# Performance work log

Measured on AMD Instinct MI355X. Metric: run time of the kernel, lower is better.

The kernel has to match this reference:

```python
import jax, jax.numpy as jnp
import numpy as np

B, S, E, L = 8, 2048, 512, 128


def setup_inputs() -> dict:
    key = jax.random.key(0)
    k1, k2 = jax.random.split(key)
    embeddings = jax.random.normal(k1, (B, S, E), dtype=jnp.float32)
    means = jax.random.normal(k2, (L, E), dtype=jnp.float32)
    var = jnp.ones((E,), dtype=jnp.float32)  # default init: requires_grad=False, ones
    return {"embeddings": embeddings, "means": means, "var": var}


def reference(embeddings, means, var):
    # Diagonal-Gaussian log-density per (token, label):
    #   log_density - 0.5 * sum_e (means[l,e] - emb[b,s,e])^2 / var[e]
    # Rewritten as GEMM + per-row/per-label norms (avoids [B,S,L,E] intermediate).
    n_embed = embeddings.shape[-1]
    factor = -n_embed / 2.0 * (np.log(2.0) + np.log(np.pi))
    # After init_params: log_density = factor - 0.5 * sum(log var); var=ones -> factor.
    log_density = factor - 0.5 * jnp.sum(jnp.log(var))
    inv_var = 1.0 / var  # [E]
    e2 = jnp.einsum('bse,e->bs', embeddings * embeddings, inv_var)      # [B,S]
    m2 = jnp.einsum('le,e->l', means * means, inv_var)                  # [L]
    cross = jnp.einsum('bse,le->bsl', embeddings, means * inv_var)      # [B,S,L]
    sq_mahalanobis = e2[..., None] + m2[None, None, :] - 2.0 * cross    # [B,S,L]
    return log_density - 0.5 * sq_mahalanobis
```

## Files before the change

### kernel.cpp

```cpp
#include <hip/hip_runtime.h>
#include <math.h>

#define BDIM 8
#define SDIM 2048
#define EDIM 512
#define LDIM 128
#define MTOT (BDIM * SDIM)
#define TM 32
#define BK 64
#define PAD 8
#define LSTR (BK + PAD)

typedef __attribute__((ext_vector_type(8))) short s8v;
typedef __attribute__((ext_vector_type(4))) float f4v;

__device__ __forceinline__ unsigned short f2bf(float x) {
    union { float f; unsigned u; } c; c.f = x;
    return (unsigned short)((c.u + 0x7fffu + ((c.u >> 16) & 1u)) >> 16);
}

__global__ __launch_bounds__(64) void gs_prep(
    const float* __restrict__ means, const float* __restrict__ var,
    unsigned short* __restrict__ Bmat, float* __restrict__ m2,
    float* __restrict__ ivbuf, float* __restrict__ coef)
{
    const int l = blockIdx.x;
    const int t = threadIdx.x;
    const int e0 = t * 8;

    float mv[8], iv[8];
    const float* mrow = means + l * EDIM + e0;
#pragma unroll
    for (int i = 0; i < 8; ++i) { mv[i] = mrow[i]; iv[i] = 1.0f / var[e0 + i]; }

    float part = 0.0f;
    s8v pr;
#pragma unroll
    for (int i = 0; i < 8; ++i) {
        float p = mv[i] * iv[i];
        pr[i] = (short)f2bf(p);
        part += mv[i] * p;
    }
    *(s8v*)(Bmat + l * EDIM + e0) = pr;

#pragma unroll
    for (int off = 32; off > 0; off >>= 1) part += __shfl_down(part, off, 64);
    if (t == 0) m2[l] = part;

    if (l == 0) {
#pragma unroll
        for (int i = 0; i < 8; ++i) ivbuf[e0 + i] = iv[i];
        float ld = 0.0f;
#pragma unroll
        for (int i = 0; i < 8; ++i) ld += logf(var[e0 + i]);
#pragma unroll
        for (int off = 32; off > 0; off >>= 1) ld += __shfl_down(ld, off, 64);
        if (t == 0) {
            const float factor = -(float)EDIM * 0.5f * 1.8378770664093453f;
            *coef = factor - 0.5f * ld;
        }
    }
}

__global__ __launch_bounds__(256) void gs_main(
    const float* __restrict__ emb, const unsigned short* __restrict__ Bmat,
    const float* __restrict__ m2, const float* __restrict__ ivbuf,
    const float* __restrict__ coef, float* __restrict__ out)
{
    __shared__ __align__(16) unsigned short Alds[TM][LSTR];
    __shared__ __align__(16) unsigned short Blds[LDIM][LSTR];
    __shared__ float e2part[256];
    __shared__ float e2s[TM];

    const int t    = threadIdx.x;
    const int lane = t & 63;
    const int wave = t >> 6;
    const int m0   = blockIdx.x * TM;

    const int arow = t >> 3;
    const int kseg = (t & 7) * 8;

    const int r0w  = (wave >> 1) * 16;
    const int c0w  = (wave & 1) * 64;
    const int frow = lane & 15;
    const int fk   = (lane >> 4) * 8;

    f4v acc[4];
#pragma unroll
    for (int i = 0; i < 4; ++i) acc[i] = (f4v)0.0f;

    float e2acc = 0.0f;
    const float* embp = emb + (m0 + arow) * EDIM + kseg;
    const unsigned short* bp = Bmat + arow * EDIM + kseg;

    for (int kc = 0; kc < EDIM / BK; ++kc) {
        const int k0 = kc * BK;
        f4v x0 = *(const f4v*)(embp + k0);
        f4v x1 = *(const f4v*)(embp + k0 + 4);
        f4v v0 = *(const f4v*)(ivbuf + k0 + kseg);
        f4v v1 = *(const f4v*)(ivbuf + k0 + kseg + 4);
        s8v b0 = *(const s8v*)(bp + (0 * 32) * EDIM + k0);
        s8v b1 = *(const s8v*)(bp + (1 * 32) * EDIM + k0);
        s8v b2 = *(const s8v*)(bp + (2 * 32) * EDIM + k0);
        s8v b3 = *(const s8v*)(bp + (3 * 32) * EDIM + k0);

        s8v a8;
#pragma unroll
        for (int i = 0; i < 4; ++i) {
            a8[i] = (short)f2bf(x0[i]);
            e2acc += x0[i] * x0[i] * v0[i];
        }
#pragma unroll
        for (int i = 0; i < 4; ++i) {
            a8[4 + i] = (short)f2bf(x1[i]);
            e2acc += x1[i] * x1[i] * v1[i];
        }

        __syncthreads();
        *(s8v*)&Alds[arow][kseg] = a8;
        *(s8v*)&Blds[arow +  0][kseg] = b0;
        *(s8v*)&Blds[arow + 32][kseg] = b1;
        *(s8v*)&Blds[arow + 64][kseg] = b2;
        *(s8v*)&Blds[arow + 96][kseg] = b3;
        __syncthreads();

#pragma unroll
        for (int ks = 0; ks < BK; ks += 32) {
            s8v af = *(const s8v*)&Alds[r0w + frow][ks + fk];
#pragma unroll
            for (int ct = 0; ct < 4; ++ct) {
                s8v bfv = *(const s8v*)&Blds[c0w + ct * 16 + frow][ks + fk];
                acc[ct] = __builtin_amdgcn_mfma_f32_16x16x32_bf16(af, bfv, acc[ct], 0, 0, 0);
            }
        }
    }

    e2part[t] = e2acc;
    __syncthreads();
    if (t < TM) {
        float s = 0.0f;
#pragma unroll
        for (int j = 0; j < 8; ++j) s += e2part[t * 8 + j];
        e2s[t] = s;
    }
    __syncthreads();

    const float cf = *coef;
#pragma unroll
    for (int ct = 0; ct < 4; ++ct) {
        const int n = c0w + ct * 16 + frow;
        const float cm = cf - 0.5f * m2[n];
#pragma unroll
        for (int r = 0; r < 4; ++r) {
            const int row = r0w + (lane >> 4) * 4 + r;
            out[(m0 + row) * LDIM + n] = acc[ct][r] + cm - 0.5f * e2s[row];
        }
    }
}

extern "C" void kernel_launch(void* const* d_in, const int* in_sizes, int n_in,
                              void* d_out, int out_size, void* d_ws, size_t ws_size,
                              hipStream_t stream) {
    const float* emb   = (const float*)d_in[0];
    const float* means = (const float*)d_in[1];
    const float* var   = (const float*)d_in[2];
    float* out = (float*)d_out;

    char* ws = (char*)d_ws;
    unsigned short* Bmat = (unsigned short*)ws;
    float* m2    = (float*)(ws + 131072);
    float* ivbuf = (float*)(ws + 131584);
    float* coef  = (float*)(ws + 133632);

    gs_prep<<<LDIM, 64, 0, stream>>>(means, var, Bmat, m2, ivbuf, coef);
    gs_main<<<MTOT / TM, 256, 0, stream>>>(emb, Bmat, m2, ivbuf, coef, out);
}
```

Measured before the change: 84.30 us.

## Pre-swizzle means into MFMA fragment layout, load B straight to registers, double-buffer A

The prep kernel now writes the scaled bf16 means matrix in the per-lane MFMA fragment order. The main kernel can then load B operands directly from global memory into registers instead of staging them through LDS. The row tile shrinks to 16 so each wave owns 32 label columns. A double-buffered LDS tile with register prefetch of the next chunk leaves one barrier per iteration, and the e2 reduction moves to shuffles. The cost is that every block re-reads the full B matrix from L2 with twice as many blocks, and there is less MFMA work per block to hide latency.

```diff
diff --git a/kernel.cpp b/kernel.cpp
--- a/kernel.cpp
+++ b/kernel.cpp
@@ -6,12 +6,13 @@
 #define EDIM 512
 #define LDIM 128
 #define MTOT (BDIM * SDIM)
-#define TM 32
+#define TM 16
 #define BK 64
-#define PAD 8
-#define LSTR (BK + PAD)
+#define NCH (EDIM / BK)
+#define LSTR 72
 
 typedef __attribute__((ext_vector_type(8))) short s8v;
+typedef __attribute__((ext_vector_type(4))) short s4v;
 typedef __attribute__((ext_vector_type(4))) float f4v;
 
 __device__ __forceinline__ unsigned short f2bf(float x) {
@@ -21,7 +22,7 @@
 
 __global__ __launch_bounds__(64) void gs_prep(
     const float* __restrict__ means, const float* __restrict__ var,
-    unsigned short* __restrict__ Bmat, float* __restrict__ m2,
+    unsigned short* __restrict__ BF, float* __restrict__ m2,
     float* __restrict__ ivbuf, float* __restrict__ coef)
 {
     const int l = blockIdx.x;
@@ -41,7 +42,9 @@
         pr[i] = (short)f2bf(p);
         part += mv[i] * p;
     }
-    *(s8v*)(Bmat + l * EDIM + e0) = pr;
+    const int ct = l >> 4, fr = l & 15;
+    const int kt = t >> 2, kg = t & 3;
+    *(s8v*)(BF + (((kt * 8 + ct) * 64) + kg * 16 + fr) * 8) = pr;
 
 #pragma unroll
     for (int off = 32; off > 0; off >>= 1) part += __shfl_down(part, off, 64);
@@ -63,13 +66,11 @@
 }
 
 __global__ __launch_bounds__(256) void gs_main(
-    const float* __restrict__ emb, const unsigned short* __restrict__ Bmat,
+    const float* __restrict__ emb, const unsigned short* __restrict__ BF,
     const float* __restrict__ m2, const float* __restrict__ ivbuf,
     const float* __restrict__ coef, float* __restrict__ out)
 {
-    __shared__ __align__(16) unsigned short Alds[TM][LSTR];
-    __shared__ __align__(16) unsigned short Blds[LDIM][LSTR];
-    __shared__ float e2part[256];
+    __shared__ __align__(16) unsigned short Alds[2][TM][LSTR];
     __shared__ float e2s[TM];
 
     const int t    = threadIdx.x;
@@ -77,84 +78,77 @@
     const int wave = t >> 6;
     const int m0   = blockIdx.x * TM;
 
-    const int arow = t >> 3;
-    const int kseg = (t & 7) * 8;
+    const int arow = t >> 4;
+    const int kq   = (t & 15) * 4;
 
-    const int r0w  = (wave >> 1) * 16;
-    const int c0w  = (wave & 1) * 64;
-    const int frow = lane & 15;
-    const int fk   = (lane >> 4) * 8;
+    const int fr = lane & 15;
+    const int kg = lane >> 4;
 
-    f4v acc[4];
+    const float* embp = emb + (m0 + arow) * EDIM + kq;
+    const unsigned short* bfp = BF + (wave * 2 * 64 + lane) * 8;
+
+    f4v acc0 = (f4v)0.0f, acc1 = (f4v)0.0f;
+    float e2acc = 0.0f;
+
+    f4v a_cur  = *(const f4v*)(embp);
+    f4v iv_cur = *(const f4v*)(ivbuf + kq);
+    s8v b00 = *(const s8v*)(bfp);
+    s8v b01 = *(const s8v*)(bfp + 512);
+    s8v b10 = *(const s8v*)(bfp + 4096);
+    s8v b11 = *(const s8v*)(bfp + 4608);
+
 #pragma unroll
-    for (int i = 0; i < 4; ++i) acc[i] = (f4v)0.0f;
-
-    float e2acc = 0.0f;
-    const float* embp = emb + (m0 + arow) * EDIM + kseg;
-    const unsigned short* bp = Bmat + arow * EDIM + kseg;
-
-    for (int kc = 0; kc < EDIM / BK; ++kc) {
-        const int k0 = kc * BK;
-        f4v x0 = *(const f4v*)(embp + k0);
-        f4v x1 = *(const f4v*)(embp + k0 + 4);
-        f4v v0 = *(const f4v*)(ivbuf + k0 + kseg);
-        f4v v1 = *(const f4v*)(ivbuf + k0 + kseg + 4);
-        s8v b0 = *(const s8v*)(bp + (0 * 32) * EDIM + k0);
-        s8v b1 = *(const s8v*)(bp + (1 * 32) * EDIM + k0);
-        s8v b2 = *(const s8v*)(bp + (2 * 32) * EDIM + k0);
-        s8v b3 = *(const s8v*)(bp + (3 * 32) * EDIM + k0);
-
-        s8v a8;
+    for (int kc = 0; kc < NCH; ++kc) {
+        s4v a4;
 #pragma unroll
         for (int i = 0; i < 4; ++i) {
-            a8[i] = (short)f2bf(x0[i]);
-            e2acc += x0[i] * x0[i] * v0[i];
+            a4[i] = (short)f2bf(a_cur[i]);
+            e2acc += a_cur[i] * a_cur[i] * iv_cur[i];
         }
-#pragma unroll
-        for (int i = 0; i < 4; ++i) {
-            a8[4 + i] = (short)f2bf(x1[i]);
-            e2acc += x1[i] * x1[i] * v1[i];
+        *(s4v*)&Alds[kc & 1][arow][kq] = a4;
+
+        f4v a_nxt, iv_nxt;
+        s8v nb00, nb01, nb10, nb11;
+        if (kc + 1 < NCH) {
+            a_nxt  = *(const f4v*)(embp + (kc + 1) * BK);
+            iv_nxt = *(const f4v*)(ivbuf + (kc + 1) * BK + kq);
+            const unsigned short* bp = bfp + (kc + 1) * 8192;
+            nb00 = *(const s8v*)(bp);
+            nb01 = *(const s8v*)(bp + 512);
+            nb10 = *(const s8v*)(bp + 4096);
+            nb11 = *(const s8v*)(bp + 4608);
         }
-
-        __syncthreads();
-        *(s8v*)&Alds[arow][kseg] = a8;
-        *(s8v*)&Blds[arow +  0][kseg] = b0;
-        *(s8v*)&Blds[arow + 32][kseg] = b1;
-        *(s8v*)&Blds[arow + 64][kseg] = b2;
-        *(s8v*)&Blds[arow + 96][kseg] = b3;
         __syncthreads();
 
-#pragma unroll
-        for (int ks = 0; ks < BK; ks += 32) {
-            s8v af = *(const s8v*)&Alds[r0w + frow][ks + fk];
-#pragma unroll
-            for (int ct = 0; ct < 4; ++ct) {
-                s8v bfv = *(const s8v*)&Blds[c0w + ct * 16 + frow][ks + fk];
-                acc[ct] = __builtin_amdgcn_mfma_f32_16x16x32_bf16(af, bfv, acc[ct], 0, 0, 0);
-            }
+        s8v af0 = *(const s8v*)&Alds[kc & 1][fr][kg * 8];
+        s8v af1 = *(const s8v*)&Alds[kc & 1][fr][32 + kg * 8];
+        acc0 = __builtin_amdgcn_mfma_f32_16x16x32_bf16(af0, b00, acc0, 0, 0, 0);
+        acc1 = __builtin_amdgcn_mfma_f32_16x16x32_bf16(af0, b01, acc1, 0, 0, 0);
+        acc0 = __builtin_amdgcn_mfma_f32_16x16x32_bf16(af1, b10, acc0, 0, 0, 0);
+        acc1 = __builtin_amdgcn_mfma_f32_16x16x32_bf16(af1, b11, acc1, 0, 0, 0);
+
+        if (kc + 1 < NCH) {
+            a_cur = a_nxt; iv_cur = iv_nxt;
+            b00 = nb00; b01 = nb01; b10 = nb10; b11 = nb11;
         }
     }
 
-    e2part[t] = e2acc;
-    __syncthreads();
-    if (t < TM) {
-        float s = 0.0f;
 #pragma unroll
-        for (int j = 0; j < 8; ++j) s += e2part[t * 8 + j];
-        e2s[t] = s;
-    }
+    for (int off = 8; off > 0; off >>= 1) e2acc += __shfl_down(e2acc, off, 16);
+    if ((t & 15) == 0) e2s[arow] = e2acc;
     __syncthreads();
 
-    const float cf = *coef;
+    const float cf  = *coef;
+    const int   n0  = wave * 32 + fr;
+    const float cm0 = cf - 0.5f * m2[n0];
+    const float cm1 = cf - 0.5f * m2[n0 + 16];
+    float* orow = out + m0 * LDIM;
 #pragma unroll
-    for (int ct = 0; ct < 4; ++ct) {
-        const int n = c0w + ct * 16 + frow;
-        const float cm = cf - 0.5f * m2[n];
-#pragma unroll
-        for (int r = 0; r < 4; ++r) {
-            const int row = r0w + (lane >> 4) * 4 + r;
-            out[(m0 + row) * LDIM + n] = acc[ct][r] + cm - 0.5f * e2s[row];
-        }
+    for (int r = 0; r < 4; ++r) {
+        const int row = kg * 4 + r;
+        const float eh = 0.5f * e2s[row];
+        orow[row * LDIM + n0]      = acc0[r] + cm0 - eh;
+        orow[row * LDIM + n0 + 16] = acc1[r] + cm1 - eh;
     }
 }
 
@@ -167,11 +161,11 @@
     float* out = (float*)d_out;
 
     char* ws = (char*)d_ws;
-    unsigned short* Bmat = (unsigned short*)ws;
+    unsigned short* BF = (unsigned short*)ws;
     float* m2    = (float*)(ws + 131072);
     float* ivbuf = (float*)(ws + 131584);
     float* coef  = (float*)(ws + 133632);
 
-    gs_prep<<<LDIM, 64, 0, stream>>>(means, var, Bmat, m2, ivbuf, coef);
-    gs_main<<<MTOT / TM, 256, 0, stream>>>(emb, Bmat, m2, ivbuf, coef, out);
+    gs_prep<<<LDIM, 64, 0, stream>>>(means, var, BF, m2, ivbuf, coef);
+    gs_main<<<MTOT / TM, 256, 0, stream>>>(emb, BF, m2, ivbuf, coef, out);
 }
```

New measurement: 83.44 us, median of 2. No clear change (-1.0%).
